# Optimization experiments

Measured on AMD Instinct MI355X. Metric: run time of the kernel, lower is better.

The kernel has to match this reference:

```python
import jax, jax.numpy as jnp
import numpy as np

D_MODEL = 512
D_STATE = 64
BATCH = 8
SEQ = 4096
LN_EPS = 1e-3  # keras LayerNormalization default epsilon


def setup_inputs() -> dict:
    key = jax.random.key(0)
    ks = jax.random.split(key, 16)
    dm, dn = D_MODEL, D_STATE
    s_dm = 1.0 / np.sqrt(dm)
    s_dn = 1.0 / np.sqrt(dn)
    return {
        "x": jax.random.normal(ks[0], (BATCH, SEQ, dm), dtype=jnp.float32),
        "ln_gamma": jnp.ones((dm,), jnp.float32),
        "ln_beta": jnp.zeros((dm,), jnp.float32),
        "W_in": jax.random.normal(ks[1], (dm, dm), jnp.float32) * s_dm,
        "b_in": jnp.zeros((dm,), jnp.float32),
        "W_xs": jax.random.normal(ks[2], (dm, dn), jnp.float32) * s_dm,
        "W_B": jax.random.normal(ks[3], (dm, dn), jnp.float32) * s_dm,
        "b_B": jnp.zeros((dn,), jnp.float32),
        "W_C": jax.random.normal(ks[4], (dm, dn), jnp.float32) * s_dm,
        "b_C": jnp.zeros((dn,), jnp.float32),
        "A_log": jax.random.uniform(ks[5], (dn,), jnp.float32, minval=-4.0, maxval=-1.0),
        "D": jnp.ones((dm,), jnp.float32),
        "W_s2o": jax.random.normal(ks[6], (dn, dm), jnp.float32) * s_dn,
        "W_out": jax.random.normal(ks[7], (dm, dm), jnp.float32) * s_dm,
        "b_out": jnp.zeros((dm,), jnp.float32),
    }


def reference(x, ln_gamma, ln_beta, W_in, b_in, W_xs, W_B, b_B, W_C, b_C,
              A_log, D, W_s2o, W_out, b_out):
    residual = x
    # LayerNorm
    mu = jnp.mean(x, axis=-1, keepdims=True)
    var = jnp.var(x, axis=-1, keepdims=True)
    xn = (x - mu) * jax.lax.rsqrt(var + LN_EPS) * ln_gamma + ln_beta
    # Projections (all per-timestep, batched as one GEMM)
    u = xn @ W_in + b_in                      # [B,S,Dm]
    Bm = u @ W_B + b_B                        # [B,S,N]
    Cm = u @ W_C + b_C                        # [B,S,N]
    xs = u @ W_xs                             # [B,S,N]
    A_bar = jnp.exp(-jnp.exp(A_log))          # [N]
    Bu = Bm * xs                              # [B,S,N] input to recurrence
    # Sequential selective scan over time (time-major)
    Bu_t = jnp.swapaxes(Bu, 0, 1)             # [S,B,N]
    C_t = jnp.swapaxes(Cm, 0, 1)              # [S,B,N]
    h0 = jnp.zeros((x.shape[0], A_log.shape[0]), dtype=x.dtype)

    def step(h, inp):
        bu, c = inp
        h = A_bar * h + bu
        return h, c * h

    _, ys = jax.lax.scan(step, h0, (Bu_t, C_t))  # ys: [S,B,N]
    ys = jnp.swapaxes(ys, 0, 1)                  # [B,S,N]
    # state_to_output is linear & time-invariant -> apply after the scan
    y = ys @ W_s2o + D * u                       # [B,S,Dm]
    y = y @ W_out + b_out
    return y + residual                          # dropout is identity at inference
```

## Files before the change

### kernel.cpp

```cpp
#include <hip/hip_runtime.h>
#include <cstddef>

typedef unsigned short u16;

constexpr int DM   = 512;
constexpr int DN   = 64;
constexpr int SEQL = 4096;
constexpr int CH   = 128;
constexpr int LCH  = SEQL / CH;
constexpr int KC   = DM + DN;

typedef __attribute__((ext_vector_type(8))) short bf16x8;
typedef __attribute__((ext_vector_type(4))) float f32x4;

__device__ inline u16 f2bf(float f) {
    unsigned int u = __float_as_uint(f);
    unsigned int r = u + 0x7FFFu + ((u >> 16) & 1u);
    return (u16)(r >> 16);
}
__device__ inline float bf2f(u16 h) {
    return __uint_as_float(((unsigned int)h) << 16);
}

__device__ inline void gload_lds16(const void* g, void* l) {
    __builtin_amdgcn_global_load_lds(
        (const __attribute__((address_space(1))) void*)g,
        (__attribute__((address_space(3))) void*)l, 16, 0, 0);
}

__global__ __launch_bounds__(256) void k_ln(const float* __restrict__ X,
                                            const float* __restrict__ gamma,
                                            const float* __restrict__ beta,
                                            u16* __restrict__ Xn) {
    const int lane = threadIdx.x & 63;
    const int w    = threadIdx.x >> 6;
    const size_t row = (size_t)blockIdx.x * 4 + w;
    const float* xr = X + row * DM;
    float4 v0 = *reinterpret_cast<const float4*>(&xr[lane * 8]);
    float4 v1 = *reinterpret_cast<const float4*>(&xr[lane * 8 + 4]);
    float s  = v0.x + v0.y + v0.z + v0.w + v1.x + v1.y + v1.z + v1.w;
    float s2 = v0.x*v0.x + v0.y*v0.y + v0.z*v0.z + v0.w*v0.w
             + v1.x*v1.x + v1.y*v1.y + v1.z*v1.z + v1.w*v1.w;
#pragma unroll
    for (int o = 32; o > 0; o >>= 1) {
        s  += __shfl_xor(s, o);
        s2 += __shfl_xor(s2, o);
    }
    const float mu = s * (1.0f / DM);
    const float rs = rsqrtf(s2 * (1.0f / DM) - mu * mu + 1e-3f);
    float4 g0 = *reinterpret_cast<const float4*>(&gamma[lane * 8]);
    float4 g1 = *reinterpret_cast<const float4*>(&gamma[lane * 8 + 4]);
    float4 b0 = *reinterpret_cast<const float4*>(&beta[lane * 8]);
    float4 b1 = *reinterpret_cast<const float4*>(&beta[lane * 8 + 4]);
    union { u16 h[8]; uint4 v; } pk;
    pk.h[0] = f2bf((v0.x - mu) * rs * g0.x + b0.x);
    pk.h[1] = f2bf((v0.y - mu) * rs * g0.y + b0.y);
    pk.h[2] = f2bf((v0.z - mu) * rs * g0.z + b0.z);
    pk.h[3] = f2bf((v0.w - mu) * rs * g0.w + b0.w);
    pk.h[4] = f2bf((v1.x - mu) * rs * g1.x + b1.x);
    pk.h[5] = f2bf((v1.y - mu) * rs * g1.y + b1.y);
    pk.h[6] = f2bf((v1.z - mu) * rs * g1.z + b1.z);
    pk.h[7] = f2bf((v1.w - mu) * rs * g1.w + b1.w);
    *reinterpret_cast<uint4*>(&Xn[row * DM + lane * 8]) = pk.v;
}

__global__ __launch_bounds__(256) void k_wtransS(const float* __restrict__ W,
                                                 u16* __restrict__ Wt,
                                                 int K, int N, int ldo,
                                                 const float* __restrict__ scale) {
    __shared__ float tile[64][65];
    const int bx = blockIdx.x, by = blockIdx.y;
    const int tx = threadIdx.x & 63, ty = threadIdx.x >> 6;
#pragma unroll
    for (int r = ty; r < 64; r += 4)
        tile[r][tx] = W[(size_t)(by * 64 + r) * N + bx * 64 + tx];
    __syncthreads();
    const float sc = scale ? scale[by * 64 + tx] : 1.0f;
#pragma unroll
    for (int r = ty; r < 64; r += 4)
        Wt[(size_t)(bx * 64 + r) * ldo + by * 64 + tx] = f2bf(sc * tile[tx][r]);
}

__global__ __launch_bounds__(256) void k_wcat(const float* __restrict__ Ws2o,
                                              const float* __restrict__ Wout,
                                              u16* __restrict__ Wcat) {
    const int tn = threadIdx.x & 63;
    const int tk = threadIdx.x >> 6;
    const int n  = blockIdx.x * 64 + tn;
    const int k  = blockIdx.y * 4 + tk;
    float s = 0.f;
#pragma unroll 8
    for (int j = 0; j < DM; ++j)
        s = fmaf(Ws2o[(size_t)k * DM + j], Wout[(size_t)j * DM + n], s);
    Wcat[(size_t)n * KC + k] = f2bf(s);
}

__global__ __launch_bounds__(256) void k_g1(const u16* __restrict__ A,
                                            const u16* __restrict__ Bt,
                                            const float* __restrict__ bias,
                                            u16* __restrict__ Out)
{
    __shared__ u16 As[2][4096];
    __shared__ u16 Bs[2][4096];
    const int tid = threadIdx.x, lane = tid & 63, w = tid >> 6;
    const int wr = w >> 1, wc = w & 1;
    int lid = blockIdx.y * gridDim.x + blockIdx.x;
    const int cpx = (gridDim.x * gridDim.y) >> 3;
    lid = (lid & 7) * cpx + (lid >> 3);
    const int n0 = (lid & 3) * 128;
    const int m0 = (lid >> 2) * 128;

    const int srow = tid >> 2, sk = (tid & 3) * 8;
    const u16* aR = A  + (size_t)(m0 + srow) * DM + sk;
    const u16* bR = Bt + (size_t)(n0 + srow) * DM + sk;
    const int kg = lane >> 4, lr = lane & 15;
    const int aoff = (wr * 64 + lr) * 32 + kg * 8;
    const int boff = (wc * 64 + lr) * 32 + kg * 8;

    f32x4 acc[4][4];
#pragma unroll
    for (int i = 0; i < 4; i++)
#pragma unroll
      for (int j = 0; j < 4; j++) acc[i][j] = (f32x4){0.f, 0.f, 0.f, 0.f};

    auto STAGE = [&](int buf, int s) {
        const u16* a0 = aR + s * 32;
        const u16* b0 = bR + s * 32;
        gload_lds16(a0,           &As[buf][w * 512]);
        gload_lds16(a0 + 64 * DM, &As[buf][2048 + w * 512]);
        gload_lds16(b0,           &Bs[buf][w * 512]);
        gload_lds16(b0 + 64 * DM, &Bs[buf][2048 + w * 512]);
    };

    STAGE(0, 0);
    __syncthreads();
    for (int s = 0; s < 16; ++s) {
        const int cur = s & 1;
        if (s + 1 < 16) STAGE(cur ^ 1, s + 1);
        bf16x8 af[4], bfr[4];
#pragma unroll
        for (int i = 0; i < 4; i++)
            af[i]  = *reinterpret_cast<const bf16x8*>(&As[cur][aoff + i * 512]);
#pragma unroll
        for (int j = 0; j < 4; j++)
            bfr[j] = *reinterpret_cast<const bf16x8*>(&Bs[cur][boff + j * 512]);
#pragma unroll
        for (int i = 0; i < 4; i++)
#pragma unroll
          for (int j = 0; j < 4; j++)
            acc[i][j] = __builtin_amdgcn_mfma_f32_16x16x32_bf16(af[i], bfr[j], acc[i][j], 0, 0, 0);
        __syncthreads();
    }

#pragma unroll
    for (int j = 0; j < 4; j++) {
        const int col = n0 + wc * 64 + j * 16 + lr;
        const float bv = bias[col];
#pragma unroll
        for (int i = 0; i < 4; i++) {
            const int rbase = m0 + wr * 64 + i * 16 + kg * 4;
#pragma unroll
            for (int r = 0; r < 4; r++)
                Out[(size_t)(rbase + r) * DM + col] = f2bf(acc[i][j][r] + bv);
        }
    }
}

__global__ __launch_bounds__(256) void k_mfma_bcx(
    const u16* __restrict__ A, const u16* __restrict__ Bt,
    const float* __restrict__ bB, const float* __restrict__ bC,
    float* __restrict__ Bu, float* __restrict__ Cc)
{
    __shared__ u16 As[2][2048];
    __shared__ u16 Bs[2][6144];
    const int tid = threadIdx.x, lane = tid & 63, w = tid >> 6;
    const int m0 = blockIdx.x * 64;

    f32x4 acc[12];
#pragma unroll
    for (int j = 0; j < 12; j++) acc[j] = (f32x4){0.f, 0.f, 0.f, 0.f};

    const int srow = tid >> 2, sk = (tid & 3) * 8;
    const u16* aR = A  + (size_t)(m0 + srow) * DM + sk;
    const u16* bR = Bt + (size_t)srow * DM + sk;
    const int kg = lane >> 4, lr = lane & 15;
    const int aoff = (w * 16 + lr) * 32 + kg * 8;

    auto STAGE = [&](int buf, int s) {
        const u16* a0 = aR + s * 32;
        const u16* b0 = bR + s * 32;
        gload_lds16(a0,            &As[buf][w * 512]);
        gload_lds16(b0,            &Bs[buf][w * 512]);
        gload_lds16(b0 + 64 * DM,  &Bs[buf][2048 + w * 512]);
        gload_lds16(b0 + 128 * DM, &Bs[buf][4096 + w * 512]);
    };

    STAGE(0, 0);
    __syncthreads();
    for (int s = 0; s < 16; ++s) {
        const int cur = s & 1;
        if (s + 1 < 16) STAGE(cur ^ 1, s + 1);
        bf16x8 af = *reinterpret_cast<const bf16x8*>(&As[cur][aoff]);
#pragma unroll
        for (int j = 0; j < 12; j++) {
            bf16x8 bfr = *reinterpret_cast<const bf16x8*>(&Bs[cur][(j * 16 + lr) * 32 + kg * 8]);
            acc[j] = __builtin_amdgcn_mfma_f32_16x16x32_bf16(af, bfr, acc[j], 0, 0, 0);
        }
        __syncthreads();
    }

#pragma unroll
    for (int j = 0; j < 4; j++) {
        const int col = j * 16 + lr;
        const float bBv = bB[col], bCv = bC[col];
#pragma unroll
        for (int r = 0; r < 4; r++) {
            const int grow = m0 + w * 16 + kg * 4 + r;
            const float xs = acc[j][r];
            const float bm = acc[j + 4][r] + bBv;
            const float cm = acc[j + 8][r] + bCv;
            Bu[(size_t)grow * DN + col] = bm * xs;
            Cc[(size_t)grow * DN + col] = cm;
        }
    }
}

__global__ void k_scan1(const float* __restrict__ Bu, const float* __restrict__ Alog,
                        float* __restrict__ Hl) {
    const int n = threadIdx.x;
    const int c = blockIdx.x;
    const int b = blockIdx.y;
    const float a = expf(-expf(Alog[n]));
    const float* p = Bu + ((size_t)(b * SEQL + c * LCH)) * DN + n;
    float h = 0.f;
#pragma unroll
    for (int t = 0; t < LCH; t++) h = fmaf(a, h, p[(size_t)t * DN]);
    Hl[(b * DN + n) * CH + c] = h;
}

__global__ void k_carry(const float* __restrict__ Hl, const float* __restrict__ Alog,
                        float* __restrict__ Hin) {
    const int i = threadIdx.x;
    const int n = i & 63;
    const float a  = expf(-expf(Alog[n]));
    const float aL = powf(a, (float)LCH);
    float hend = 0.f;
    for (int c = 0; c < CH; c++) {
        Hin[(size_t)i * CH + c] = hend;
        hend = fmaf(aL, hend, Hl[(size_t)i * CH + c]);
    }
}

__global__ void k_scan2(const float* __restrict__ Bu, const float* __restrict__ Cc,
                        const float* __restrict__ Hin, const float* __restrict__ Alog,
                        u16* __restrict__ Ysb) {
    const int n = threadIdx.x;
    const int c = blockIdx.x;
    const int b = blockIdx.y;
    const float a = expf(-expf(Alog[n]));
    float h = Hin[((size_t)(b * DN + n)) * CH + c];
    const size_t base = ((size_t)(b * SEQL + c * LCH)) * DN + n;
#pragma unroll
    for (int t = 0; t < LCH; t++) {
        h = fmaf(a, h, Bu[base + (size_t)t * DN]);
        Ysb[base + (size_t)t * DN] = f2bf(Cc[base + (size_t)t * DN] * h);
    }
}

__global__ __launch_bounds__(256) void k_gfuse(
    const u16* __restrict__ Ysb, const u16* __restrict__ Ub,
    const u16* __restrict__ Wcat, const float* __restrict__ bias,
    const float* __restrict__ X, float* __restrict__ Out)
{
    __shared__ u16 As[2][4096];
    __shared__ u16 Bs[2][4096];
    const int tid = threadIdx.x, lane = tid & 63, w = tid >> 6;
    const int wr = w >> 1, wc = w & 1;
    int lid = blockIdx.y * gridDim.x + blockIdx.x;
    const int cpx = (gridDim.x * gridDim.y) >> 3;
    lid = (lid & 7) * cpx + (lid >> 3);
    const int n0 = (lid & 3) * 128;
    const int m0 = (lid >> 2) * 128;

    const int srow = tid >> 2, sk = (tid & 3) * 8;
    const u16* aY = Ysb + (size_t)(m0 + srow) * DN + sk;
    const u16* aU = Ub  + (size_t)(m0 + srow) * DM + sk;
    const u16* bR = Wcat + (size_t)(n0 + srow) * KC + sk;
    const int kg = lane >> 4, lr = lane & 15;
    const int aoff = (wr * 64 + lr) * 32 + kg * 8;
    const int boff = (wc * 64 + lr) * 32 + kg * 8;

    f32x4 acc[4][4];
#pragma unroll
    for (int i = 0; i < 4; i++)
#pragma unroll
      for (int j = 0; j < 4; j++) acc[i][j] = (f32x4){0.f, 0.f, 0.f, 0.f};

    auto STAGE = [&](int buf, int s) {
        const u16 *a0, *a1;
        if (s < 2) { a0 = aY + s * 32;       a1 = a0 + 64 * DN; }
        else       { a0 = aU + (s - 2) * 32; a1 = a0 + 64 * DM; }
        const u16* b0 = bR + s * 32;
        gload_lds16(a0,           &As[buf][w * 512]);
        gload_lds16(a1,           &As[buf][2048 + w * 512]);
        gload_lds16(b0,           &Bs[buf][w * 512]);
        gload_lds16(b0 + 64 * KC, &Bs[buf][2048 + w * 512]);
    };

    STAGE(0, 0);
    __syncthreads();
    for (int s = 0; s < 18; ++s) {
        const int cur = s & 1;
        if (s + 1 < 18) STAGE(cur ^ 1, s + 1);
        bf16x8 af[4], bfr[4];
#pragma unroll
        for (int i = 0; i < 4; i++)
            af[i]  = *reinterpret_cast<const bf16x8*>(&As[cur][aoff + i * 512]);
#pragma unroll
        for (int j = 0; j < 4; j++)
            bfr[j] = *reinterpret_cast<const bf16x8*>(&Bs[cur][boff + j * 512]);
#pragma unroll
        for (int i = 0; i < 4; i++)
#pragma unroll
          for (int j = 0; j < 4; j++)
            acc[i][j] = __builtin_amdgcn_mfma_f32_16x16x32_bf16(af[i], bfr[j], acc[i][j], 0, 0, 0);
        __syncthreads();
    }

#pragma unroll
    for (int j = 0; j < 4; j++) {
        const int col = n0 + wc * 64 + j * 16 + lr;
        const float bv = bias[col];
#pragma unroll
        for (int i = 0; i < 4; i++) {
            const int rbase = m0 + wr * 64 + i * 16 + kg * 4;
#pragma unroll
            for (int r = 0; r < 4; r++) {
                const size_t idx = (size_t)(rbase + r) * DM + col;
                Out[idx] = acc[i][j][r] + bv + X[idx];
            }
        }
    }
}

extern "C" void kernel_launch(void* const* d_in, const int* in_sizes, int n_in,
                              void* d_out, int out_size, void* d_ws, size_t ws_size,
                              hipStream_t stream) {
    const float* X     = (const float*)d_in[0];
    const float* gamma = (const float*)d_in[1];
    const float* beta  = (const float*)d_in[2];
    const float* W_in  = (const float*)d_in[3];
    const float* b_in  = (const float*)d_in[4];
    const float* W_xs  = (const float*)d_in[5];
    const float* W_B   = (const float*)d_in[6];
    const float* b_B   = (const float*)d_in[7];
    const float* W_C   = (const float*)d_in[8];
    const float* b_C   = (const float*)d_in[9];
    const float* A_log = (const float*)d_in[10];
    const float* Dv    = (const float*)d_in[11];
    const float* W_s2o = (const float*)d_in[12];
    const float* W_out = (const float*)d_in[13];
    const float* b_out = (const float*)d_in[14];
    float* out = (float*)d_out;

    const int M = in_sizes[0] / DM;
    const int B = M / SEQL;

    float* ws  = (float*)d_ws;
    float* Bu  = ws;
    float* Cc  = Bu + (size_t)M * DN;
    float* Hl  = Cc + (size_t)M * DN;
    float* Hin = Hl + (size_t)B * DN * CH;
    u16* Xn    = (u16*)(Hin + (size_t)B * DN * CH);
    u16* Ub    = Xn + (size_t)M * DM;
    u16* Ysb   = Ub + (size_t)M * DM;
    u16* WinT  = Ysb + (size_t)M * DN;
    u16* WbcxT = WinT + (size_t)DM * DM;
    u16* WcatT = WbcxT + (size_t)3 * DN * DM;

    k_ln<<<M / 4, 256, 0, stream>>>(X, gamma, beta, Xn);
    k_wtransS<<<dim3(8, 8), 256, 0, stream>>>(W_in, WinT, DM, DM, DM, nullptr);
    k_wtransS<<<dim3(1, 8), 256, 0, stream>>>(W_xs, WbcxT,            DM, DN, DM, nullptr);
    k_wtransS<<<dim3(1, 8), 256, 0, stream>>>(W_B,  WbcxT + 64 * DM,  DM, DN, DM, nullptr);
    k_wtransS<<<dim3(1, 8), 256, 0, stream>>>(W_C,  WbcxT + 128 * DM, DM, DN, DM, nullptr);
    k_wtransS<<<dim3(8, 8), 256, 0, stream>>>(W_out, WcatT + 64, DM, DM, KC, Dv);
    k_wcat<<<dim3(8, 16), 256, 0, stream>>>(W_s2o, W_out, WcatT);

    k_g1<<<dim3(4, M / 128), 256, 0, stream>>>(Xn, WinT, b_in, Ub);
    k_mfma_bcx<<<dim3(M / 64), 256, 0, stream>>>(Ub, WbcxT, b_B, b_C, Bu, Cc);
    k_scan1<<<dim3(CH, B), 64, 0, stream>>>(Bu, A_log, Hl);
    k_carry<<<1, B * DN, 0, stream>>>(Hl, A_log, Hin);
    k_scan2<<<dim3(CH, B), 64, 0, stream>>>(Bu, Cc, Hin, A_log, Ysb);
    k_gfuse<<<dim3(4, M / 128), 256, 0, stream>>>(Ysb, Ub, WcatT, b_out, X, out);
}
```

Baseline: 174.1 us.

## Restructure output GEMM to keep weight slice resident in LDS and stream A

```diff
diff --git a/kernel.cpp b/kernel.cpp
--- a/kernel.cpp
+++ b/kernel.cpp
@@ -267,77 +267,70 @@
     }
 }
 
-__global__ __launch_bounds__(256) void k_gfuse(
+__global__ __launch_bounds__(256) void k_gfuse_stream(
     const u16* __restrict__ Ysb, const u16* __restrict__ Ub,
     const u16* __restrict__ Wcat, const float* __restrict__ bias,
     const float* __restrict__ X, float* __restrict__ Out)
 {
-    __shared__ u16 As[2][4096];
-    __shared__ u16 Bs[2][4096];
+    constexpr int LDB = 584;
+    __shared__ u16 Bsh[32 * LDB];
     const int tid = threadIdx.x, lane = tid & 63, w = tid >> 6;
     const int wr = w >> 1, wc = w & 1;
-    int lid = blockIdx.y * gridDim.x + blockIdx.x;
-    const int cpx = (gridDim.x * gridDim.y) >> 3;
-    lid = (lid & 7) * cpx + (lid >> 3);
-    const int n0 = (lid & 3) * 128;
-    const int m0 = (lid >> 2) * 128;
-
-    const int srow = tid >> 2, sk = (tid & 3) * 8;
-    const u16* aY = Ysb + (size_t)(m0 + srow) * DN + sk;
-    const u16* aU = Ub  + (size_t)(m0 + srow) * DM + sk;
-    const u16* bR = Wcat + (size_t)(n0 + srow) * KC + sk;
+    const int bid = blockIdx.x;
+    const int t      = bid >> 3;
+    const int nblk   = t & 15;
+    const int stripe = (bid & 7) + 8 * (t >> 4);
+    const int n0     = nblk * 32;
+
+    {
+        const int col = tid & 31, q = tid >> 5;
+        const u16* src = Wcat + (size_t)(n0 + col) * KC;
+#pragma unroll
+        for (int r = 0; r < 9; ++r) {
+            const int chunk = q + r * 8;
+            const uint4 v = *reinterpret_cast<const uint4*>(src + chunk * 8);
+            *reinterpret_cast<uint4*>(&Bsh[col * LDB + chunk * 8]) = v;
+        }
+    }
+    __syncthreads();
+
     const int kg = lane >> 4, lr = lane & 15;
-    const int aoff = (wr * 64 + lr) * 32 + kg * 8;
-    const int boff = (wc * 64 + lr) * 32 + kg * 8;
-
-    f32x4 acc[4][4];
-#pragma unroll
-    for (int i = 0; i < 4; i++)
-#pragma unroll
-      for (int j = 0; j < 4; j++) acc[i][j] = (f32x4){0.f, 0.f, 0.f, 0.f};
-
-    auto STAGE = [&](int buf, int s) {
-        const u16 *a0, *a1;
-        if (s < 2) { a0 = aY + s * 32;       a1 = a0 + 64 * DN; }
-        else       { a0 = aU + (s - 2) * 32; a1 = a0 + 64 * DM; }
-        const u16* b0 = bR + s * 32;
-        gload_lds16(a0,           &As[buf][w * 512]);
-        gload_lds16(a1,           &As[buf][2048 + w * 512]);
-        gload_lds16(b0,           &Bs[buf][w * 512]);
-        gload_lds16(b0 + 64 * KC, &Bs[buf][2048 + w * 512]);
-    };
-
-    STAGE(0, 0);
-    __syncthreads();
-    for (int s = 0; s < 18; ++s) {
-        const int cur = s & 1;
-        if (s + 1 < 18) STAGE(cur ^ 1, s + 1);
-        bf16x8 af[4], bfr[4];
-#pragma unroll
-        for (int i = 0; i < 4; i++)
-            af[i]  = *reinterpret_cast<const bf16x8*>(&As[cur][aoff + i * 512]);
-#pragma unroll
-        for (int j = 0; j < 4; j++)
-            bfr[j] = *reinterpret_cast<const bf16x8*>(&Bs[cur][boff + j * 512]);
-#pragma unroll
-        for (int i = 0; i < 4; i++)
-#pragma unroll
-          for (int j = 0; j < 4; j++)
-            acc[i][j] = __builtin_amdgcn_mfma_f32_16x16x32_bf16(af[i], bfr[j], acc[i][j], 0, 0, 0);
-        __syncthreads();
-    }
-
-#pragma unroll
-    for (int j = 0; j < 4; j++) {
-        const int col = n0 + wc * 64 + j * 16 + lr;
+    const int bbase = (wc * 16 + lr) * LDB + kg * 8;
+
+    for (int mt = 0; mt < 4; ++mt) {
+        const int m0 = stripe * 512 + mt * 128;
+        f32x4 acc[4];
+#pragma unroll
+        for (int i = 0; i < 4; i++) acc[i] = (f32x4){0.f, 0.f, 0.f, 0.f};
+
+        const u16* aY0 = Ysb + (size_t)(m0 + wr * 64 + lr) * DN + kg * 8;
+        const u16* aU0 = Ub  + (size_t)(m0 + wr * 64 + lr) * DM + kg * 8;
+
+#pragma unroll
+        for (int ks = 0; ks < 18; ++ks) {
+            bf16x8 af[4];
+#pragma unroll
+            for (int i = 0; i < 4; ++i) {
+                if (ks < 2)
+                    af[i] = *reinterpret_cast<const bf16x8*>(aY0 + (size_t)(i * 16) * DN + ks * 32);
+                else
+                    af[i] = *reinterpret_cast<const bf16x8*>(aU0 + (size_t)(i * 16) * DM + (ks - 2) * 32);
+            }
+            const bf16x8 bf0 = *reinterpret_cast<const bf16x8*>(&Bsh[bbase + ks * 32]);
+#pragma unroll
+            for (int i = 0; i < 4; ++i)
+                acc[i] = __builtin_amdgcn_mfma_f32_16x16x32_bf16(af[i], bf0, acc[i], 0, 0, 0);
+        }
+
+        const int col = n0 + wc * 16 + lr;
         const float bv = bias[col];
 #pragma unroll
-        for (int i = 0; i < 4; i++) {
+        for (int i = 0; i < 4; ++i) {
             const int rbase = m0 + wr * 64 + i * 16 + kg * 4;
 #pragma unroll
-            for (int r = 0; r < 4; r++) {
+            for (int r = 0; r < 4; ++r) {
                 const size_t idx = (size_t)(rbase + r) * DM + col;
-                Out[idx] = acc[i][j][r] + bv + X[idx];
+                Out[idx] = acc[i][r] + bv + X[idx];
             }
         }
     }
@@ -391,5 +384,5 @@
     k_scan1<<<dim3(CH, B), 64, 0, stream>>>(Bu, A_log, Hl);
     k_carry<<<1, B * DN, 0, stream>>>(Hl, A_log, Hin);
     k_scan2<<<dim3(CH, B), 64, 0, stream>>>(Bu, Cc, Hin, A_log, Ysb);
-    k_gfuse<<<dim3(4, M / 128), 256, 0, stream>>>(Ysb, Ub, WcatT, b_out, X, out);
-}
+    k_gfuse_stream<<<1024, 256, 0, stream>>>(Ysb, Ub, WcatT, b_out, X, out);
+}
```

Result: slower. 273.4 us (+57.1%).
